# Kernel tuning notes

Measured on AMD Instinct MI355X. Metric: run time of the kernel, lower is better.

Reference implementation:

```python
import jax, jax.numpy as jnp
import numpy as np

B, N, NC, T, C, H = 8, 16, 16, 64, 512, 8


def setup_inputs() -> dict:
    key = jax.random.key(0)
    ks = jax.random.split(key, 7)
    s = 1.0 / np.sqrt(C)  # ~kaiming-uniform scale for Linear weights
    x = jax.random.normal(ks[0], (B, N, T, C), dtype=jnp.float32)
    c = jax.random.normal(ks[1], (B, NC, T, C), dtype=jnp.float32)
    mask = jax.random.randint(ks[2], (B, N * T, (N + NC) * T), 0, 2).astype(bool)
    Wq = jax.random.normal(ks[3], (C, C), dtype=jnp.float32) * s  # [out, in], torch Linear layout
    Wk = jax.random.normal(ks[4], (C, C), dtype=jnp.float32) * s
    Wv = jax.random.normal(ks[5], (C, C), dtype=jnp.float32) * s
    Wp = jax.random.normal(ks[6], (C, C), dtype=jnp.float32) * s
    return {"x": x, "c": c, "mask": mask, "Wq": Wq, "Wk": Wk, "Wv": Wv, "Wp": Wp}


def reference(x, c, mask, Wq, Wk, Wv, Wp):
    Bx, Nx, Tx, Cx = x.shape
    Dh = Cx // H
    kv_in = jnp.concatenate([x, c], axis=1)           # hybrid: [B, N+NC, T, C]
    Nk = kv_in.shape[1]
    # torch Linear: y = x @ W.T  -> einsum '...c,dc->...d'
    q = jnp.einsum('bntc,dc->bntd', x, Wq).reshape(Bx, Nx * Tx, H, Dh).transpose(0, 2, 1, 3)
    k = jnp.einsum('bntc,dc->bntd', kv_in, Wk).reshape(Bx, Nk * Tx, H, Dh).transpose(0, 2, 1, 3)
    v = jnp.einsum('bntc,dc->bntd', kv_in, Wv).reshape(Bx, Nk * Tx, H, Dh).transpose(0, 2, 1, 3)
    att = jnp.einsum('bhqd,bhkd->bhqk', q, k) * (1.0 / np.sqrt(Dh))  # [B,H,NT,NkT]
    att = jnp.where(mask[:, None, :, :], -jnp.inf, att)
    att = jax.nn.softmax(att, axis=-1)
    y = jnp.einsum('bhqk,bhkd->bhqd', att, v)          # [B,H,NT,Dh]
    y = y.transpose(0, 2, 1, 3).reshape(Bx, Nx * Tx, Cx)
    y = jnp.einsum('btc,dc->btd', y, Wp)
    return y.reshape(Bx, Nx, Tx, Cx)
```

## Files before the change

### kernel.cpp

```cpp
#include <hip/hip_runtime.h>
#include <hip/hip_bf16.h>
#include <stdint.h>

typedef __bf16 v8bf __attribute__((ext_vector_type(8)));
typedef short v4s __attribute__((ext_vector_type(4)));
typedef float f32x4 __attribute__((ext_vector_type(4)));

__device__ __forceinline__ void gload_lds16(const void* g, void* l) {
    __builtin_amdgcn_global_load_lds(
        (const __attribute__((address_space(1))) void*)g,
        (__attribute__((address_space(3))) void*)l, 16, 0, 0);
}

__device__ __forceinline__ unsigned short f2bf(float f) {
    __hip_bfloat16 h = __float2bfloat16(f);
    return __builtin_bit_cast(unsigned short, h);
}

__device__ __forceinline__ float andf(float e, int m) {
    return __builtin_bit_cast(float, __builtin_bit_cast(unsigned int, e) & (unsigned int)m);
}

#if __has_builtin(__builtin_amdgcn_sbfe)
#define SBIT(w, off, ioff) __builtin_amdgcn_sbfe((int)(w), (unsigned)(off), 1u)
#else
#define SBIT(w, off, ioff) (((int)((w) << (ioff))) >> 31)
#endif

__device__ __forceinline__ f32x4 mfma16x16x16bf(v4s a, v4s b, f32x4 c) {
#if __has_builtin(__builtin_amdgcn_mfma_f32_16x16x16bf16_1k)
    return __builtin_amdgcn_mfma_f32_16x16x16bf16_1k(a, b, c, 0, 0, 0);
#elif __has_builtin(__builtin_amdgcn_mfma_f32_16x16x16_bf16)
    return __builtin_amdgcn_mfma_f32_16x16x16_bf16(a, b, c, 0, 0, 0);
#else
    asm("s_nop 1\n\t"
        "v_mfma_f32_16x16x16_bf16 %0, %1, %2, %0\n\t"
        "s_nop 7\n\ts_nop 3"
        : "+v"(c) : "v"(a), "v"(b));
    return c;
#endif
}

__global__ __launch_bounds__(256) void cvt_xcw(const float* __restrict__ x,
                                               const float* __restrict__ c,
                                               const float* __restrict__ wq,
                                               const float* __restrict__ wk,
                                               const float* __restrict__ wv,
                                               const float* __restrict__ wp,
                                               __hip_bfloat16* __restrict__ xc,
                                               __hip_bfloat16* __restrict__ wout) {
    int bid = blockIdx.x;
    if (bid < 8192) {
        int i = bid * 256 + threadIdx.x;
        long e = (long)i * 4;
        int b = (int)(e >> 20);
        int rem = (int)(e & ((1 << 20) - 1));
        int r = rem >> 9;
        int col = rem & 511;
        const float* src = (r < 1024) ? (x + ((long)b << 19) + (long)r * 512 + col)
                                      : (c + ((long)b << 19) + (long)(r - 1024) * 512 + col);
        float4 v = *(const float4*)src;
        ushort4 o;
        o.x = f2bf(v.x); o.y = f2bf(v.y); o.z = f2bf(v.z); o.w = f2bf(v.w);
        ((ushort4*)xc)[i] = o;
    } else {
        int i = (bid - 8192) * 256 + threadIdx.x;
        int e = i * 4;
        int w = e >> 18;
        int off = e & ((1 << 18) - 1);
        const float* src = (w == 0 ? wq : w == 1 ? wk : w == 2 ? wv : wp) + off;
        float4 val = *(const float4*)src;
        ushort4 o;
        o.x = f2bf(val.x); o.y = f2bf(val.y); o.z = f2bf(val.z); o.w = f2bf(val.w);
        ((ushort4*)wout)[i] = o;
    }
}

__global__ __launch_bounds__(256) void cvt_mask(const int* __restrict__ mask,
                                                unsigned long long* __restrict__ mbt) {
    int t = threadIdx.x;
    long base = (long)blockIdx.x * 1024;
#pragma unroll
    for (int j = 0; j < 4; j++) {
        long i = base + j * 256 + t;
        int v = mask[i] != 0;
        unsigned long long bits = __ballot(v);
        if ((t & 63) == 0) {
            int b = (int)(i >> 21);
            int q = (int)((i >> 11) & 1023);
            int word = (int)((i >> 6) & 31);
            mbt[((long)b * 32 + word) * 1024 + q] = bits;
        }
    }
}

__global__ __launch_bounds__(256) void gemm_qkv(const __hip_bfloat16* __restrict__ A,
                                                const __hip_bfloat16* __restrict__ Bw,
                                                __hip_bfloat16* __restrict__ Qw,
                                                __hip_bfloat16* __restrict__ Kw,
                                                __hip_bfloat16* __restrict__ Vtw) {
    __shared__ union {
        struct { __hip_bfloat16 As[2][128 * 32]; __hip_bfloat16 Bs[2][128 * 32]; } s;
        __hip_bfloat16 T[64 * 136];
    } u;
    const int tid = threadIdx.x;
    const int wave = tid >> 6, lane = tid & 63;
    const int m0 = blockIdx.x * 128, n0 = blockIdx.y * 128;

    const int la = lane >> 2;
    const int kc = (lane & 3) * 8;
    const long ga0 = (long)(m0 + wave * 16 + la) * 512 + kc;
    const long ga1 = (long)(m0 + (wave + 4) * 16 + la) * 512 + kc;
    const long gb0 = (long)(n0 + wave * 16 + la) * 512 + kc;
    const long gb1 = (long)(n0 + (wave + 4) * 16 + la) * 512 + kc;

    f32x4 acc[4][4] = {};
    const int mw = (wave & 1) * 64, nw = (wave >> 1) * 64;
    const int lrow = lane & 15, lk = (lane >> 4) * 8;

    gload_lds16(A + ga0, &u.s.As[0][wave * 512]);
    gload_lds16(A + ga1, &u.s.As[0][(wave + 4) * 512]);
    gload_lds16(Bw + gb0, &u.s.Bs[0][wave * 512]);
    gload_lds16(Bw + gb1, &u.s.Bs[0][(wave + 4) * 512]);
    __syncthreads();

    for (int it = 0; it < 16; ++it) {
        const int cur = it & 1;
        if (it < 15) {
            const int k0 = (it + 1) * 32;
            gload_lds16(A + ga0 + k0, &u.s.As[cur ^ 1][wave * 512]);
            gload_lds16(A + ga1 + k0, &u.s.As[cur ^ 1][(wave + 4) * 512]);
            gload_lds16(Bw + gb0 + k0, &u.s.Bs[cur ^ 1][wave * 512]);
            gload_lds16(Bw + gb1 + k0, &u.s.Bs[cur ^ 1][(wave + 4) * 512]);
        }
        v8bf a[4], b[4];
#pragma unroll
        for (int i = 0; i < 4; i++) {
            a[i] = *(const v8bf*)&u.s.As[cur][(mw + i * 16 + lrow) * 32 + lk];
            b[i] = *(const v8bf*)&u.s.Bs[cur][(nw + i * 16 + lrow) * 32 + lk];
        }
        __builtin_amdgcn_s_setprio(1);
#pragma unroll
        for (int mi = 0; mi < 4; mi++)
#pragma unroll
            for (int ni = 0; ni < 4; ni++)
                acc[mi][ni] = __builtin_amdgcn_mfma_f32_16x16x32_bf16(a[mi], b[ni], acc[mi][ni], 0, 0, 0);
        __builtin_amdgcn_s_setprio(0);
        __syncthreads();
    }

    const int lq = lane >> 4;
    if (blockIdx.y < 8) {
#pragma unroll
        for (int mi = 0; mi < 4; mi++)
#pragma unroll
            for (int ni = 0; ni < 4; ni++)
#pragma unroll
                for (int r = 0; r < 4; r++) {
                    int grow = m0 + mw + mi * 16 + lq * 4 + r;
                    int gcol = n0 + nw + ni * 16 + lrow;
                    int w = gcol >> 9, g9 = gcol & 511;
                    int h = g9 >> 6, dh = g9 & 63;
                    int b_ = grow >> 11, rr = grow & 2047;
                    float val = acc[mi][ni][r];
                    if (w == 0) {
                        if (rr < 1024)
                            Qw[((long)(b_ * 8 + h) * 1024 + rr) * 64 + dh] =
                                __float2bfloat16(val * 0.1803368801f);
                    } else {
                        Kw[((long)(b_ * 8 + h) * 2048 + rr) * 64 + dh] = __float2bfloat16(val);
                    }
                }
    } else {
        const int no = (blockIdx.y - 8) * 128;
        const int b_ = m0 >> 11, rrb = m0 & 2047;
#pragma unroll
        for (int pass = 0; pass < 2; ++pass) {
            __syncthreads();
            if ((wave >> 1) == pass) {
#pragma unroll
                for (int mi = 0; mi < 4; mi++)
#pragma unroll
                    for (int ni = 0; ni < 4; ni++) {
                        int n_l = ni * 16 + lrow;
                        int m_l = mw + mi * 16 + lq * 4;
                        ushort4 pk;
                        pk.x = f2bf(acc[mi][ni][0]); pk.y = f2bf(acc[mi][ni][1]);
                        pk.z = f2bf(acc[mi][ni][2]); pk.w = f2bf(acc[mi][ni][3]);
                        *(ushort4*)&u.T[n_l * 136 + m_l] = pk;
                    }
            }
            __syncthreads();
#pragma unroll
            for (int i = 0; i < 4; i++) {
                int sI = tid + i * 256;
                int n_l = sI >> 4, ch = sI & 15;
                int ng = no + pass * 64 + n_l;
                int h = ng >> 6, dh = ng & 63;
                uint4 v = *(const uint4*)&u.T[n_l * 136 + ch * 8];
                *(uint4*)&Vtw[((long)(b_ * 8 + h) * 64 + dh) * 2048 + rrb + ch * 8] = v;
            }
        }
    }
}

__global__ __launch_bounds__(256) void gemm_out(const __hip_bfloat16* __restrict__ A,
                                                const __hip_bfloat16* __restrict__ Bw,
                                                float* __restrict__ outp) {
    __shared__ __hip_bfloat16 As[2][128 * 32];
    __shared__ __hip_bfloat16 Bs[2][128 * 32];
    const int tid = threadIdx.x;
    const int wave = tid >> 6, lane = tid & 63;
    const int m0 = blockIdx.x * 128, n0 = blockIdx.y * 128;

    const int la = lane >> 2;
    const int kc = (lane & 3) * 8;
    const long ga0 = (long)(m0 + wave * 16 + la) * 512 + kc;
    const long ga1 = (long)(m0 + (wave + 4) * 16 + la) * 512 + kc;
    const long gb0 = (long)(n0 + wave * 16 + la) * 512 + kc;
    const long gb1 = (long)(n0 + (wave + 4) * 16 + la) * 512 + kc;

    f32x4 acc[4][4] = {};
    const int mw = (wave & 1) * 64, nw = (wave >> 1) * 64;
    const int lrow = lane & 15, lk = (lane >> 4) * 8;

    gload_lds16(A + ga0, &As[0][wave * 512]);
    gload_lds16(A + ga1, &As[0][(wave + 4) * 512]);
    gload_lds16(Bw + gb0, &Bs[0][wave * 512]);
    gload_lds16(Bw + gb1, &Bs[0][(wave + 4) * 512]);
    __syncthreads();

    for (int it = 0; it < 16; ++it) {
        const int cur = it & 1;
        if (it < 15) {
            const int k0 = (it + 1) * 32;
            gload_lds16(A + ga0 + k0, &As[cur ^ 1][wave * 512]);
            gload_lds16(A + ga1 + k0, &As[cur ^ 1][(wave + 4) * 512]);
            gload_lds16(Bw + gb0 + k0, &Bs[cur ^ 1][wave * 512]);
            gload_lds16(Bw + gb1 + k0, &Bs[cur ^ 1][(wave + 4) * 512]);
        }
        v8bf a[4], b[4];
#pragma unroll
        for (int i = 0; i < 4; i++) {
            a[i] = *(const v8bf*)&As[cur][(mw + i * 16 + lrow) * 32 + lk];
            b[i] = *(const v8bf*)&Bs[cur][(nw + i * 16 + lrow) * 32 + lk];
        }
        __builtin_amdgcn_s_setprio(1);
#pragma unroll
        for (int mi = 0; mi < 4; mi++)
#pragma unroll
            for (int ni = 0; ni < 4; ni++)
                acc[mi][ni] = __builtin_amdgcn_mfma_f32_16x16x32_bf16(a[mi], b[ni], acc[mi][ni], 0, 0, 0);
        __builtin_amdgcn_s_setprio(0);
        __syncthreads();
    }

    const int lq = lane >> 4;
#pragma unroll
    for (int mi = 0; mi < 4; mi++)
#pragma unroll
        for (int ni = 0; ni < 4; ni++)
#pragma unroll
            for (int r = 0; r < 4; r++) {
                int grow = m0 + mw + mi * 16 + lq * 4 + r;
                int gcol = n0 + nw + ni * 16 + lrow;
                outp[(long)grow * 512 + gcol] = acc[mi][ni][r];
            }
}

__global__ __launch_bounds__(256) void flash(const __hip_bfloat16* __restrict__ Q,
                                             const __hip_bfloat16* __restrict__ K,
                                             const __hip_bfloat16* __restrict__ Vt,
                                             const unsigned long long* __restrict__ Mbt,
                                             __hip_bfloat16* __restrict__ Y) {
    constexpr int LDT = 72;
    __shared__ __hip_bfloat16 Ks[2][64 * LDT];
    __shared__ __hip_bfloat16 Vts[2][64 * LDT];

    const int L = blockIdx.x;
    const int b = L & 7, qt = (L >> 3) & 15, h = L >> 7;
    const int bh = b * 8 + h;
    const int tid = threadIdx.x, w = tid >> 6, lane = tid & 63;
    const int lcol = lane & 15, lq = lane >> 4;

    const __hip_bfloat16* Qp = Q + ((long)bh * 1024 + qt * 64 + w * 16 + lcol) * 64 + lq * 8;
    const __hip_bfloat16* Kg = K + (long)bh * 2048 * 64;
    const __hip_bfloat16* Vg = Vt + (long)bh * 64 * 2048;
    const unsigned long long* Mp = Mbt + (long)b * 32 * 1024 + qt * 64 + w * 16 + lcol;

    const int u0 = tid, u1 = tid + 256;
    const int r0 = u0 >> 3, p0 = u0 & 7;
    const int r1 = u1 >> 3, p1 = u1 & 7;

    int boff[8], ioff[8];
#pragma unroll
    for (int jj = 0; jj < 8; jj++) {
        boff[jj] = (jj >> 2) * 16 + lq * 4 + (jj & 3);
        ioff[jj] = 31 - boff[jj];
    }

    v8bf bq0 = *(const v8bf*)(Qp);
    v8bf bq1 = *(const v8bf*)(Qp + 32);

    f32x4 O[4] = {};
    float lsum = 0.f;

    unsigned long long mword = Mp[0];
    {
        const uint4* ksrc = (const uint4*)Kg;
        uint4 k0 = ksrc[u0], k1 = ksrc[u1];
        uint4 v0 = *(const uint4*)(Vg + (long)r0 * 2048 + p0 * 8);
        uint4 v1 = *(const uint4*)(Vg + (long)r1 * 2048 + p1 * 8);
        *(uint4*)&Ks[0][r0 * LDT + p0 * 8] = k0;
        *(uint4*)&Ks[0][r1 * LDT + p1 * 8] = k1;
        *(uint4*)&Vts[0][r0 * LDT + p0 * 8] = v0;
        *(uint4*)&Vts[0][r1 * LDT + p1 * 8] = v1;
    }
    __syncthreads();

    int cur = 0;
    for (int kt = 0; kt < 32; kt++) {
        const unsigned int kw_lo = ~(unsigned int)mword;
        const unsigned int kw_hi = ~(unsigned int)(mword >> 32);

        uint4 nk0, nk1, nv0, nv1;
        if (kt < 31) {
            const uint4* ksrc = (const uint4*)(Kg + ((kt + 1) << 12));
            nk0 = ksrc[u0];
            nk1 = ksrc[u1];
            nv0 = *(const uint4*)(Vg + (long)r0 * 2048 + (kt + 1) * 64 + p0 * 8);
            nv1 = *(const uint4*)(Vg + (long)r1 * 2048 + (kt + 1) * 64 + p1 * 8);
            mword = Mp[(long)(kt + 1) * 1024];
        }

        const __hip_bfloat16* Kb = Ks[cur];
        const __hip_bfloat16* Vb = Vts[cur];
#pragma unroll
        for (int nt = 0; nt < 4; nt++) {
            v8bf ak0 = *(const v8bf*)&Kb[(nt * 16 + lcol) * LDT + lq * 8];
            v8bf ak1 = *(const v8bf*)&Kb[(nt * 16 + lcol) * LDT + 32 + lq * 8];
            f32x4 st = {};
            __builtin_amdgcn_s_setprio(1);
            st = __builtin_amdgcn_mfma_f32_16x16x32_bf16(ak0, bq0, st, 0, 0, 0);
            st = __builtin_amdgcn_mfma_f32_16x16x32_bf16(ak1, bq1, st, 0, 0, 0);
            __builtin_amdgcn_s_setprio(0);
            const unsigned int kw = (nt < 2) ? kw_lo : kw_hi;
            const int base = (nt & 1) * 4;
            float e0 = andf(__builtin_amdgcn_exp2f(st[0]), SBIT(kw, boff[base + 0], ioff[base + 0]));
            float e1 = andf(__builtin_amdgcn_exp2f(st[1]), SBIT(kw, boff[base + 1], ioff[base + 1]));
            float e2 = andf(__builtin_amdgcn_exp2f(st[2]), SBIT(kw, boff[base + 2], ioff[base + 2]));
            float e3 = andf(__builtin_amdgcn_exp2f(st[3]), SBIT(kw, boff[base + 3], ioff[base + 3]));
            lsum += (e0 + e1) + (e2 + e3);
            __hip_bfloat162 lo = __float22bfloat162_rn(make_float2(e0, e1));
            __hip_bfloat162 hi = __float22bfloat162_rn(make_float2(e2, e3));
            uint2 pku;
            __builtin_memcpy(&pku.x, &lo, 4);
            __builtin_memcpy(&pku.y, &hi, 4);
            v4s pa = __builtin_bit_cast(v4s, pku);
            __builtin_amdgcn_s_setprio(1);
#pragma unroll
            for (int nd = 0; nd < 4; nd++) {
                v4s bv = *(const v4s*)&Vb[(nd * 16 + lcol) * LDT + nt * 16 + lq * 4];
                O[nd] = mfma16x16x16bf(pa, bv, O[nd]);
            }
            __builtin_amdgcn_s_setprio(0);
        }

        if (kt < 31) {
            __hip_bfloat16* Kw_ = Ks[cur ^ 1];
            __hip_bfloat16* Vw_ = Vts[cur ^ 1];
            *(uint4*)&Kw_[r0 * LDT + p0 * 8] = nk0;
            *(uint4*)&Kw_[r1 * LDT + p1 * 8] = nk1;
            *(uint4*)&Vw_[r0 * LDT + p0 * 8] = nv0;
            *(uint4*)&Vw_[r1 * LDT + p1 * 8] = nv1;
        }
        __syncthreads();
        cur ^= 1;
    }

    float s = lsum;
    s += __shfl_xor(s, 16);
    s += __shfl_xor(s, 32);
    float inv[4];
#pragma unroll
    for (int r = 0; r < 4; r++) inv[r] = 1.f / __shfl(s, lq * 4 + r);

    __hip_bfloat16* Yp = Y + ((long)b * 1024 + qt * 64 + w * 16) * 512 + h * 64 + lcol;
#pragma unroll
    for (int nd = 0; nd < 4; nd++)
#pragma unroll
        for (int r = 0; r < 4; r++)
            Yp[(long)(lq * 4 + r) * 512 + nd * 16] = __float2bfloat16(O[nd][r] * inv[r]);
}

extern "C" void kernel_launch(void* const* d_in, const int* in_sizes, int n_in,
                              void* d_out, int out_size, void* d_ws, size_t ws_size,
                              hipStream_t stream) {
    const float* x = (const float*)d_in[0];
    const float* c = (const float*)d_in[1];
    const int* mask = (const int*)d_in[2];
    const float* Wq = (const float*)d_in[3];
    const float* Wk = (const float*)d_in[4];
    const float* Wv = (const float*)d_in[5];
    const float* Wp = (const float*)d_in[6];

    char* ws = (char*)d_ws;
    __hip_bfloat16* xc  = (__hip_bfloat16*)(ws);
    __hip_bfloat16* Wbf = (__hip_bfloat16*)(ws + 16777216);
    __hip_bfloat16* Qw  = (__hip_bfloat16*)(ws + 18874368);
    __hip_bfloat16* Kw  = (__hip_bfloat16*)(ws + 27262976);
    __hip_bfloat16* Vtw = (__hip_bfloat16*)(ws + 44040192);
    __hip_bfloat16* Yb  = (__hip_bfloat16*)(ws + 60817408);
    unsigned long long* Mbp = (unsigned long long*)(ws);

    cvt_xcw<<<9216, 256, 0, stream>>>(x, c, Wq, Wk, Wv, Wp, xc, Wbf);
    gemm_qkv<<<dim3(128, 12), 256, 0, stream>>>(xc, Wbf, Qw, Kw, Vtw);
    cvt_mask<<<16384, 256, 0, stream>>>(mask, Mbp);
    flash<<<1024, 256, 0, stream>>>(Qw, Kw, Vtw, Mbp, Yb);
    gemm_out<<<dim3(64, 4), 256, 0, stream>>>(Yb, Wbf + 3 * 262144, (float*)d_out);
}
```

Measured before the change: 268.2 us.

## Use explicit vmcnt barriers in GEMMs and MFMA row-sum in flash attention

In both projection GEMMs, the __syncthreads pairs are replaced with inline s_waitcnt vmcnt(4)/s_barrier so only the older LDS-bound loads are waited on, which keeps the prefetch in flight during compute. In the flash kernel, the softmax denominator now comes from an extra MFMA against a ones vector instead of scalar adds and cross-lane shuffles. The mask bit extract always uses the shift form. This adds one MFMA per tile and relies on the hand-written waitcnt counts being correct for the direct-to-LDS loads. The row sum is also now taken over bf16-rounded probabilities, so it matches the values fed to the PV product.

```diff
diff --git a/kernel.cpp b/kernel.cpp
--- a/kernel.cpp
+++ b/kernel.cpp
@@ -21,11 +21,11 @@
     return __builtin_bit_cast(float, __builtin_bit_cast(unsigned int, e) & (unsigned int)m);
 }
 
-#if __has_builtin(__builtin_amdgcn_sbfe)
-#define SBIT(w, off, ioff) __builtin_amdgcn_sbfe((int)(w), (unsigned)(off), 1u)
-#else
 #define SBIT(w, off, ioff) (((int)((w) << (ioff))) >> 31)
-#endif
+
+#define WAITV4_BAR() asm volatile("s_waitcnt vmcnt(4)\n\ts_barrier" ::: "memory")
+#define WAITV0_BAR() asm volatile("s_waitcnt vmcnt(0)\n\ts_barrier" ::: "memory")
+#define RAW_BAR() asm volatile("s_barrier" ::: "memory")
 
 __device__ __forceinline__ f32x4 mfma16x16x16bf(v4s a, v4s b, f32x4 c) {
 #if __has_builtin(__builtin_amdgcn_mfma_f32_16x16x16bf16_1k)
@@ -122,7 +122,6 @@
     gload_lds16(A + ga1, &u.s.As[0][(wave + 4) * 512]);
     gload_lds16(Bw + gb0, &u.s.Bs[0][wave * 512]);
     gload_lds16(Bw + gb1, &u.s.Bs[0][(wave + 4) * 512]);
-    __syncthreads();
 
     for (int it = 0; it < 16; ++it) {
         const int cur = it & 1;
@@ -132,6 +131,9 @@
             gload_lds16(A + ga1 + k0, &u.s.As[cur ^ 1][(wave + 4) * 512]);
             gload_lds16(Bw + gb0 + k0, &u.s.Bs[cur ^ 1][wave * 512]);
             gload_lds16(Bw + gb1 + k0, &u.s.Bs[cur ^ 1][(wave + 4) * 512]);
+            WAITV4_BAR();
+        } else {
+            WAITV0_BAR();
         }
         v8bf a[4], b[4];
 #pragma unroll
@@ -146,7 +148,7 @@
             for (int ni = 0; ni < 4; ni++)
                 acc[mi][ni] = __builtin_amdgcn_mfma_f32_16x16x32_bf16(a[mi], b[ni], acc[mi][ni], 0, 0, 0);
         __builtin_amdgcn_s_setprio(0);
-        __syncthreads();
+        RAW_BAR();
     }
 
     const int lq = lane >> 4;
@@ -228,7 +230,6 @@
     gload_lds16(A + ga1, &As[0][(wave + 4) * 512]);
     gload_lds16(Bw + gb0, &Bs[0][wave * 512]);
     gload_lds16(Bw + gb1, &Bs[0][(wave + 4) * 512]);
-    __syncthreads();
 
     for (int it = 0; it < 16; ++it) {
         const int cur = it & 1;
@@ -238,6 +239,9 @@
             gload_lds16(A + ga1 + k0, &As[cur ^ 1][(wave + 4) * 512]);
             gload_lds16(Bw + gb0 + k0, &Bs[cur ^ 1][wave * 512]);
             gload_lds16(Bw + gb1 + k0, &Bs[cur ^ 1][(wave + 4) * 512]);
+            WAITV4_BAR();
+        } else {
+            WAITV0_BAR();
         }
         v8bf a[4], b[4];
 #pragma unroll
@@ -252,7 +256,7 @@
             for (int ni = 0; ni < 4; ni++)
                 acc[mi][ni] = __builtin_amdgcn_mfma_f32_16x16x32_bf16(a[mi], b[ni], acc[mi][ni], 0, 0, 0);
         __builtin_amdgcn_s_setprio(0);
-        __syncthreads();
+        RAW_BAR();
     }
 
     const int lq = lane >> 4;
@@ -292,18 +296,17 @@
     const int r0 = u0 >> 3, p0 = u0 & 7;
     const int r1 = u1 >> 3, p1 = u1 & 7;
 
-    int boff[8], ioff[8];
-#pragma unroll
-    for (int jj = 0; jj < 8; jj++) {
-        boff[jj] = (jj >> 2) * 16 + lq * 4 + (jj & 3);
-        ioff[jj] = 31 - boff[jj];
-    }
+    int ioff[8];
+#pragma unroll
+    for (int jj = 0; jj < 8; jj++)
+        ioff[jj] = 31 - ((jj >> 2) * 16 + lq * 4 + (jj & 3));
 
     v8bf bq0 = *(const v8bf*)(Qp);
     v8bf bq1 = *(const v8bf*)(Qp + 32);
 
     f32x4 O[4] = {};
-    float lsum = 0.f;
+    f32x4 Osum = {};
+    const v4s bones = {(short)0x3F80, (short)0x3F80, (short)0x3F80, (short)0x3F80};
 
     unsigned long long mword = Mp[0];
     {
@@ -346,11 +349,10 @@
             __builtin_amdgcn_s_setprio(0);
             const unsigned int kw = (nt < 2) ? kw_lo : kw_hi;
             const int base = (nt & 1) * 4;
-            float e0 = andf(__builtin_amdgcn_exp2f(st[0]), SBIT(kw, boff[base + 0], ioff[base + 0]));
-            float e1 = andf(__builtin_amdgcn_exp2f(st[1]), SBIT(kw, boff[base + 1], ioff[base + 1]));
-            float e2 = andf(__builtin_amdgcn_exp2f(st[2]), SBIT(kw, boff[base + 2], ioff[base + 2]));
-            float e3 = andf(__builtin_amdgcn_exp2f(st[3]), SBIT(kw, boff[base + 3], ioff[base + 3]));
-            lsum += (e0 + e1) + (e2 + e3);
+            float e0 = andf(__builtin_amdgcn_exp2f(st[0]), SBIT(kw, , ioff[base + 0]));
+            float e1 = andf(__builtin_amdgcn_exp2f(st[1]), SBIT(kw, , ioff[base + 1]));
+            float e2 = andf(__builtin_amdgcn_exp2f(st[2]), SBIT(kw, , ioff[base + 2]));
+            float e3 = andf(__builtin_amdgcn_exp2f(st[3]), SBIT(kw, , ioff[base + 3]));
             __hip_bfloat162 lo = __float22bfloat162_rn(make_float2(e0, e1));
             __hip_bfloat162 hi = __float22bfloat162_rn(make_float2(e2, e3));
             uint2 pku;
@@ -358,6 +360,7 @@
             __builtin_memcpy(&pku.y, &hi, 4);
             v4s pa = __builtin_bit_cast(v4s, pku);
             __builtin_amdgcn_s_setprio(1);
+            Osum = mfma16x16x16bf(pa, bones, Osum);
 #pragma unroll
             for (int nd = 0; nd < 4; nd++) {
                 v4s bv = *(const v4s*)&Vb[(nd * 16 + lcol) * LDT + nt * 16 + lq * 4];
@@ -378,12 +381,9 @@
         cur ^= 1;
     }
 
-    float s = lsum;
-    s += __shfl_xor(s, 16);
-    s += __shfl_xor(s, 32);
     float inv[4];
 #pragma unroll
-    for (int r = 0; r < 4; r++) inv[r] = 1.f / __shfl(s, lq * 4 + r);
+    for (int r = 0; r < 4; r++) inv[r] = 1.f / Osum[r];
 
     __hip_bfloat16* Yp = Y + ((long)b * 1024 + qt * 64 + w * 16) * 512 + h * 64 + lcol;
 #pragma unroll
```

Result: faster. 262.1 us (-2.3%).
